# Optimization experiments

Hardware: AMD Instinct MI355X
Metric: run time of the kernel (lower is better)

The kernel has to match this reference:

```python
import jax, jax.numpy as jnp
import numpy as np

B, T, O, H, CTX, HOR = 32, 24, 128, 512, 256, 48
MAX_STEP = 2.0


def setup_inputs() -> dict:
    key = jax.random.key(0)
    ks = jax.random.split(key, 20)
    def lin(k, out_d, in_d):
        bound = 1.0 / np.sqrt(in_d)
        kw, kb = jax.random.split(k)
        W = jax.random.uniform(kw, (out_d, in_d), jnp.float32, -bound, bound)
        b = jax.random.uniform(kb, (out_d,), jnp.float32, -bound, bound)
        return W, b
    W_emb, b_emb = lin(ks[0], H, 2)
    W_ctx, b_ctx = lin(ks[1], H, CTX)
    Wi_enc, bi_enc = lin(ks[2], 3 * H, H)
    Wh_enc, bh_enc = lin(ks[3], 3 * H, H)
    Wi_cell, bi_cell = lin(ks[4], 3 * H, H)
    Wh_cell, bh_cell = lin(ks[5], 3 * H, H)
    W1, b1 = lin(ks[6], H, H)
    W2, b2 = lin(ks[7], 2, H)
    z_ctx = jax.random.normal(ks[8], (B, CTX), jnp.float32)
    traj_hist = jax.random.uniform(ks[9], (B, T, O, 2), jnp.float32) * 10.0
    return dict(z_ctx=z_ctx, traj_hist=traj_hist,
                W_emb=W_emb, b_emb=b_emb, W_ctx=W_ctx, b_ctx=b_ctx,
                Wi_enc=Wi_enc, Wh_enc=Wh_enc, bi_enc=bi_enc, bh_enc=bh_enc,
                Wi_cell=Wi_cell, Wh_cell=Wh_cell, bi_cell=bi_cell, bh_cell=bh_cell,
                W1=W1, b1=b1, W2=W2, b2=b2, horizon=HOR)


def _gru(h, x, Wi, Wh, bi, bh):
    # PyTorch GRU gate math: gates ordered (r, z, n)
    gi = x @ Wi.T + bi  # [N, 3H]
    gh = h @ Wh.T + bh
    ir, iz, inn = jnp.split(gi, 3, axis=-1)
    hr, hz, hn = jnp.split(gh, 3, axis=-1)
    r = jax.nn.sigmoid(ir + hr)
    z = jax.nn.sigmoid(iz + hz)
    n = jnp.tanh(inn + r * hn)
    return (1.0 - z) * n + z * h


def reference(z_ctx, traj_hist, W_emb, b_emb, W_ctx, b_ctx,
              Wi_enc, Wh_enc, bi_enc, bh_enc,
              Wi_cell, Wh_cell, bi_cell, bh_cell,
              W1, b1, W2, b2, horizon):
    b, t, o, _ = traj_hist.shape
    Hd = W_emb.shape[0]
    seq = traj_hist.transpose(0, 2, 1, 3).reshape(b * o, t, 2)  # [N, t, 2]
    emb = seq @ W_emb.T + b_emb  # [N, t, H]

    h0 = jnp.zeros((b * o, Hd), traj_hist.dtype)
    def enc_step(h, x):
        return _gru(h, x, Wi_enc, Wh_enc, bi_enc, bh_enc), None
    h, _ = jax.lax.scan(enc_step, h0, emb.transpose(1, 0, 2))

    ctx = z_ctx @ W_ctx.T + b_ctx                         # [b, H]
    ctx = jnp.repeat(ctx[:, None, :], o, axis=1).reshape(b * o, Hd)
    h = h + ctx

    state0 = seq[:, -1]  # [N, 2]
    def dec_step(carry, _):
        h, state = carry
        inp = state @ W_emb.T + b_emb
        h = _gru(h, inp, Wi_cell, Wh_cell, bi_cell, bh_cell)
        d = jax.nn.gelu(h @ W1.T + b1, approximate=False) @ W2.T + b2  # [N, 2]
        d = MAX_STEP * jnp.tanh(d / MAX_STEP)
        s = state + d
        state = jnp.stack([jnp.clip(s[..., 0], -90.0, 90.0),
                           jnp.mod(s[..., 1], 360.0)], axis=-1)
        return (h, state), state
    _, outs = jax.lax.scan(dec_step, (h, state0), None, length=horizon)
    # outs: [horizon, N, 2] -> [b, horizon, o, 2]
    return outs.transpose(1, 0, 2).reshape(b, o, horizon, 2).transpose(0, 2, 1, 3)
```

## Files before the change

kernel.cpp:

```cpp
#include <hip/hip_runtime.h>
#include <hip/hip_bf16.h>
#include <math.h>

#define BB 32
#define TT 24
#define OO 128
#define HH 512
#define CTXD 256
#define HOR 48
#define NN (BB*OO)
#define G3 (3*HH)
#define KS 17

typedef unsigned short ushortt;
typedef __attribute__((ext_vector_type(8))) short bf16x8;
typedef __attribute__((ext_vector_type(4))) float f32x4;

__device__ __forceinline__ ushortt f2bf(float x) {
    union { float f; unsigned u; } v; v.f = x;
    unsigned r = v.u + 0x7FFF + ((v.u >> 16) & 1);
    return (ushortt)(r >> 16);
}
__device__ __forceinline__ float bf2f(ushortt b) {
    union { unsigned u; float f; } v; v.u = ((unsigned)b) << 16;
    return v.f;
}
__device__ __forceinline__ void splitbf(float x, ushortt& hi, ushortt& lo) {
    hi = f2bf(x);
    lo = f2bf(x - bf2f(hi));
}
__device__ __forceinline__ float sigm(float x) { return 1.f / (1.f + __expf(-x)); }
__device__ __forceinline__ float tanh_fast(float x) {
    float xc = fminf(fmaxf(x, -10.f), 10.f);
    float e = __expf(2.f * xc);
    return (e - 1.f) / (e + 1.f);
}


#define STEP_LOADA(Ad, ksv) do { const unsigned ko = (unsigned)(ksv) * 512; \
  _Pragma("unroll") for (int m_ = 0; m_ < 2; m_++) { \
    Ad[m_*2+0] = *reinterpret_cast<const bf16x8*>(RAh + ao[m_] + ko); \
    Ad[m_*2+1] = *reinterpret_cast<const bf16x8*>(RAl + ao[m_] + ko); \
  } } while(0)
#define STEP_LOADB(Bd, ksv) do { const unsigned ko = (unsigned)(ksv) * 512; \
  _Pragma("unroll") for (int i_ = 0; i_ < 6; i_++) { \
    Bd[i_*2+0] = *reinterpret_cast<const bf16x8*>(Bh + bo[i_] + ko); \
    Bd[i_*2+1] = *reinterpret_cast<const bf16x8*>(Bl + bo[i_] + ko); \
  } } while(0)
#define STEP_MFMA(Av, Bv) do { \
  _Pragma("unroll") for (int m_ = 0; m_ < 2; m_++) \
  _Pragma("unroll") for (int i_ = 0; i_ < 6; i_++) \
    acc[m_][i_] = __builtin_amdgcn_mfma_f32_16x16x32_bf16(Av[m_*2+0], Bv[i_*2+0], acc[m_][i_], 0,0,0); \
  _Pragma("unroll") for (int m_ = 0; m_ < 2; m_++) \
  _Pragma("unroll") for (int i_ = 0; i_ < 6; i_++) \
    acc[m_][i_] = __builtin_amdgcn_mfma_f32_16x16x32_bf16(Av[m_*2+0], Bv[i_*2+1], acc[m_][i_], 0,0,0); \
  _Pragma("unroll") for (int m_ = 0; m_ < 2; m_++) \
  _Pragma("unroll") for (int i_ = 0; i_ < 6; i_++) \
    acc[m_][i_] = __builtin_amdgcn_mfma_f32_16x16x32_bf16(Av[m_*2+1], Bv[i_*2+0], acc[m_][i_], 0,0,0); \
  } while(0)

template<bool ENC>
__global__ __launch_bounds__(256, 2) void step_kernel(
    const ushortt* __restrict__ RAh, const ushortt* __restrict__ RAl,
    ushortt* __restrict__ WAh, ushortt* __restrict__ WAl,
    const ushortt* __restrict__ Bh, const ushortt* __restrict__ Bl,
    const float* __restrict__ U, const float* __restrict__ cin,
    const float* __restrict__ xsrc, int t, const float* __restrict__ ctx)
{
    __shared__ float hbuf[128 * 36];
    const int mb = blockIdx.x & 31;
    const int jb = blockIdx.x >> 5;
    const int w = threadIdx.x >> 6, lane = threadIdx.x & 63;
    const int quad = lane >> 4, l15 = lane & 15;
    const int mtg = mb * 8 + w * 2;

    f32x4 acc[2][6];
#pragma unroll
    for (int a = 0; a < 2; a++)
#pragma unroll
        for (int b = 0; b < 6; b++) acc[a][b] = (f32x4){0.f,0.f,0.f,0.f};

    unsigned ao[2], bo[6];
#pragma unroll
    for (int mt = 0; mt < 2; mt++) ao[mt] = (unsigned)(mtg + mt) * (KS*512) + lane * 8;
#pragma unroll
    for (int g = 0; g < 3; g++)
#pragma unroll
        for (int jt = 0; jt < 2; jt++)
            bo[g*2+jt] = (unsigned)(g*32 + jb*2 + jt) * (KS*512) + lane * 8;

    bf16x8 aC[4], bC[12], aN[4], bN[12];
    STEP_LOADA(aC, 0); STEP_LOADB(bC, 0);
#pragma unroll 1
    for (int ks = 0; ks < 16; ks += 2) {
        STEP_LOADA(aN, ks+1); STEP_LOADB(bN, ks+1);
        STEP_MFMA(aC, bC);
        STEP_LOADA(aC, ks+2); STEP_LOADB(bC, ks+2);
        STEP_MFMA(aN, bN);
    }
    STEP_MFMA(aC, bC);

    const int jlo = jb * 32;
    float u0[2], u1[2], cc[2];
#pragma unroll
    for (int jt = 0; jt < 2; jt++) {
        int j = jlo + jt*16 + l15;
        u0[jt] = U[(1024 + j) * 2];
        u1[jt] = U[(1024 + j) * 2 + 1];
        cc[jt] = cin[1024 + j];
    }
    float x0v[2][4], x1v[2][4];
#pragma unroll
    for (int mt = 0; mt < 2; mt++)
#pragma unroll
        for (int reg = 0; reg < 4; reg++) {
            int row = (mtg + mt) * 16 + quad * 4 + reg;
            const float* p;
            if (ENC) p = xsrc + (((size_t)(row >> 7) * TT + t) * OO + (row & 127)) * 2;
            else     p = xsrc + (size_t)row * 2;
            x0v[mt][reg] = p[0]; x1v[mt][reg] = p[1];
        }
#pragma unroll
    for (int mt = 0; mt < 2; mt++)
#pragma unroll
        for (int jt = 0; jt < 2; jt++) {
            int qk = jt*2 + (l15 >> 3), slot = l15 & 7;
#pragma unroll
            for (int reg = 0; reg < 4; reg++) {
                int row = (mtg + mt) * 16 + quad * 4 + reg;
                float pr = acc[mt][0*2+jt][reg];
                float pz = acc[mt][1*2+jt][reg];
                float hn = acc[mt][2*2+jt][reg];
                unsigned pos = ((unsigned)((mtg + mt) * KS + jb) * 64 + qk*16 + quad*4 + reg) * 8 + slot;
                float hold = bf2f(RAh[pos]) + bf2f(RAl[pos]);
                float inn = fmaf(x1v[mt][reg], u1[jt], fmaf(x0v[mt][reg], u0[jt], cc[jt]));
                float rg = sigm(pr), zg = sigm(pz);
                float nn = tanh_fast(inn + rg * hn);
                float h = (1.f - zg) * nn + zg * hold;
                if (ENC && t == TT - 1) h += ctx[(size_t)(row >> 7) * HH + jlo + jt*16 + l15];
                hbuf[(w*32 + mt*16 + quad*4 + reg) * 36 + jt*16 + l15] = h;
            }
        }
    __syncthreads();
#pragma unroll
    for (int rr = 0; rr < 2; rr++) {
        int fr = threadIdx.x + 256 * rr;
        int mt8 = fr >> 6, fl = fr & 63;
        int qk = fl >> 4, rloc = mt8 * 16 + (fl & 15);
        const float4 v0 = *reinterpret_cast<const float4*>(&hbuf[rloc * 36 + qk * 8]);
        const float4 v1 = *reinterpret_cast<const float4*>(&hbuf[rloc * 36 + qk * 8 + 4]);
        float src[8] = {v0.x, v0.y, v0.z, v0.w, v1.x, v1.y, v1.z, v1.w};
        bf16x8 hv, lv;
#pragma unroll
        for (int s = 0; s < 8; s++) {
            ushortt hi, lo; splitbf(src[s], hi, lo);
            hv[s] = (short)hi; lv[s] = (short)lo;
        }
        unsigned base = ((unsigned)((mb*8 + mt8) * KS + jb) * 64 + fl) * 8;
        *reinterpret_cast<bf16x8*>(WAh + base) = hv;
        *reinterpret_cast<bf16x8*>(WAl + base) = lv;
    }
    if (ENC && jb == 0 && threadIdx.x < 128) {
        int row = mb * 128 + threadIdx.x;
        int tn = (t < TT - 1) ? (t + 1) : (TT - 1);
        const float* p = xsrc + (((size_t)(row >> 7) * TT + tn) * OO + (row & 127)) * 2;
        ushortt h0, l0, h1, l1;
        splitbf(p[0], h0, l0); splitbf(p[1], h1, l1);
        unsigned xb = ((unsigned)((row >> 4) * KS + 16) * 64 + (row & 15)) * 8;
        WAh[xb + 0] = h0; WAl[xb + 0] = l0;
        WAh[xb + 1] = h1; WAl[xb + 1] = l1;
    }
}

#define HEAD_LOADA(Ad, ksv) do { const unsigned ko = (unsigned)(ksv) * 512; \
  _Pragma("unroll") for (int m_ = 0; m_ < 2; m_++) { \
    Ad[m_*2+0] = *reinterpret_cast<const bf16x8*>(Ah + hao[m_] + ko); \
    Ad[m_*2+1] = *reinterpret_cast<const bf16x8*>(Al + hao[m_] + ko); \
  } } while(0)
#define HEAD_LOADB(Bd, ksv) do { const unsigned ko = (unsigned)(ksv) * 512; \
  _Pragma("unroll") for (int n_ = 0; n_ < 2; n_++) { \
    Bd[n_*2+0] = *reinterpret_cast<const bf16x8*>(Bh + hbo[n_] + ko); \
    Bd[n_*2+1] = *reinterpret_cast<const bf16x8*>(Bl + hbo[n_] + ko); \
  } } while(0)
#define HEAD_MFMA(Av, Bv) do { \
  _Pragma("unroll") for (int m_ = 0; m_ < 2; m_++) \
  _Pragma("unroll") for (int n_ = 0; n_ < 2; n_++) { \
    acc[m_][n_] = __builtin_amdgcn_mfma_f32_16x16x32_bf16(Av[m_*2+0], Bv[n_*2+0], acc[m_][n_], 0,0,0); \
    acc[m_][n_] = __builtin_amdgcn_mfma_f32_16x16x32_bf16(Av[m_*2+0], Bv[n_*2+1], acc[m_][n_], 0,0,0); \
    acc[m_][n_] = __builtin_amdgcn_mfma_f32_16x16x32_bf16(Av[m_*2+1], Bv[n_*2+0], acc[m_][n_], 0,0,0); \
  } } while(0)

__global__ __launch_bounds__(256, 2) void head_kernel(
    ushortt* Ah, ushortt* Al,
    const ushortt* __restrict__ Bh, const ushortt* __restrict__ Bl,
    const float* __restrict__ W2, const float* __restrict__ b2,
    float* __restrict__ d, unsigned* __restrict__ ctr,
    float* state, float* __restrict__ out, int t)
{
    const int mb = blockIdx.x & 31;
    const int nb = blockIdx.x >> 5;
    const int w = threadIdx.x >> 6, lane = threadIdx.x & 63;
    const int quad = lane >> 4, l15 = lane & 15;
    const int mtg = mb * 8 + w * 2;

    f32x4 acc[2][2];
#pragma unroll
    for (int a = 0; a < 2; a++)
#pragma unroll
        for (int b = 0; b < 2; b++) acc[a][b] = (f32x4){0.f,0.f,0.f,0.f};

    unsigned hao[2], hbo[2];
#pragma unroll
    for (int mt = 0; mt < 2; mt++) hao[mt] = (unsigned)(mtg + mt) * (KS*512) + lane * 8;
#pragma unroll
    for (int nt = 0; nt < 2; nt++) hbo[nt] = (unsigned)(nb*2 + nt) * (KS*512) + lane * 8;

    bf16x8 aC[4], bC[4], aN[4], bN[4];
    HEAD_LOADA(aC, 0); HEAD_LOADB(bC, 0);
#pragma unroll 1
    for (int ks = 0; ks < 16; ks += 2) {
        HEAD_LOADA(aN, ks+1); HEAD_LOADB(bN, ks+1);
        HEAD_MFMA(aC, bC);
        HEAD_LOADA(aC, ks+2); HEAD_LOADB(bC, ks+2);
        HEAD_MFMA(aN, bN);
    }
    HEAD_MFMA(aC, bC);

    float w2a[2], w2b[2];
#pragma unroll
    for (int nt = 0; nt < 2; nt++) {
        int col = (nb*2 + nt) * 16 + l15;
        w2a[nt] = W2[col]; w2b[nt] = W2[HH + col];
    }
    float p0[2][4], p1[2][4];
#pragma unroll
    for (int mt = 0; mt < 2; mt++)
#pragma unroll
        for (int reg = 0; reg < 4; reg++) { p0[mt][reg] = 0.f; p1[mt][reg] = 0.f; }
#pragma unroll
    for (int mt = 0; mt < 2; mt++)
#pragma unroll
        for (int nt = 0; nt < 2; nt++)
#pragma unroll
            for (int reg = 0; reg < 4; reg++) {
                float v = acc[mt][nt][reg];
                v = 0.5f * v * (1.0f + erff(v * 0.70710678118654752440f));
                p0[mt][reg] = fmaf(v, w2a[nt], p0[mt][reg]);
                p1[mt][reg] = fmaf(v, w2b[nt], p1[mt][reg]);
            }
#pragma unroll
    for (int m = 1; m < 16; m <<= 1)
#pragma unroll
        for (int mt = 0; mt < 2; mt++)
#pragma unroll
            for (int reg = 0; reg < 4; reg++) {
                p0[mt][reg] += __shfl_xor(p0[mt][reg], m, 64);
                p1[mt][reg] += __shfl_xor(p1[mt][reg], m, 64);
            }
    if (l15 == 0) {
#pragma unroll
        for (int mt = 0; mt < 2; mt++)
#pragma unroll
            for (int reg = 0; reg < 4; reg++) {
                int row = (mtg + mt) * 16 + quad * 4 + reg;
                atomicAdd(&d[row * 2], p0[mt][reg]);
                atomicAdd(&d[row * 2 + 1], p1[mt][reg]);
            }
    }

    __syncthreads();
    __shared__ unsigned lastv;
    if (threadIdx.x == 0) lastv = atomicAdd(ctr, 1u);
    __syncthreads();
    if (lastv == 511) {
        __threadfence();
#pragma unroll 1
        for (int rr = 0; rr < 16; rr++) {
            int row = rr * 256 + threadIdx.x;
            float d0 = d[row * 2]     + b2[0];
            float d1 = d[row * 2 + 1] + b2[1];
            d0 = 2.0f * tanhf(d0 * 0.5f);
            d1 = 2.0f * tanhf(d1 * 0.5f);
            float s0 = state[row * 2] + d0;
            s0 = fminf(fmaxf(s0, -90.f), 90.f);
            float s1 = state[row * 2 + 1] + d1;
            float rrm = fmodf(s1, 360.f);
            if (rrm < 0.f) rrm += 360.f;
            state[row * 2] = s0; state[row * 2 + 1] = rrm;
            float* op = out + (((size_t)(row >> 7) * HOR + t) * OO + (row & 127)) * 2;
            op[0] = s0; op[1] = rrm;
            ushortt h0, l0, h1, l1;
            splitbf(s0, h0, l0); splitbf(rrm, h1, l1);
            unsigned xb = ((unsigned)((row >> 4) * KS + 16) * 64 + (row & 15)) * 8;
            Ah[xb + 0] = h0; Al[xb + 0] = l0;
            Ah[xb + 1] = h1; Al[xb + 1] = l1;
        }
    }
}

__global__ __launch_bounds__(256) void fuse_kernel(
    const float* __restrict__ Wi_enc, const float* __restrict__ bi_enc,
    const float* __restrict__ Wi_cell, const float* __restrict__ bi_cell,
    const float* __restrict__ W_emb, const float* __restrict__ b_emb,
    float* __restrict__ Ue, float* __restrict__ ce,
    float* __restrict__ Ud, float* __restrict__ cd) {
    int w = threadIdx.x >> 6, lane = threadIdx.x & 63;
    int gidx = blockIdx.x * 4 + w;
    int which = gidx >= G3;
    int j = gidx - which * G3;
    const float* Wi = which ? Wi_cell : Wi_enc;
    const float* bi = which ? bi_cell : bi_enc;
    float u0 = 0.f, u1 = 0.f, cc = 0.f;
#pragma unroll
    for (int i = 0; i < 8; i++) {
        int k = i * 64 + lane;
        float wv = Wi[(size_t)j * HH + k];
        u0 = fmaf(wv, W_emb[2*k],   u0);
        u1 = fmaf(wv, W_emb[2*k+1], u1);
        cc = fmaf(wv, b_emb[k],     cc);
    }
#pragma unroll
    for (int m = 1; m < 64; m <<= 1) {
        u0 += __shfl_xor(u0, m, 64);
        u1 += __shfl_xor(u1, m, 64);
        cc += __shfl_xor(cc, m, 64);
    }
    if (lane == 0) {
        float* Uo = which ? Ud : Ue;
        float* cv = which ? cd : ce;
        Uo[j * 2 + 0] = u0; Uo[j * 2 + 1] = u1; cv[j] = cc + bi[j];
    }
}

__global__ void pack_frag(const float* __restrict__ W, const float* __restrict__ bhv,
                          const float* __restrict__ U, const float* __restrict__ cin,
                          const float* __restrict__ b1,
                          ushortt* __restrict__ Fh, ushortt* __restrict__ Fl, int N) {
    int idx = blockIdx.x * 256 + threadIdx.x;
    if (idx >= N * KS * 4) return;
    int n = idx / (KS * 4);
    int rem = idx - n * (KS * 4);
    int ks = rem >> 2, quad = rem & 3;
    int nt = n >> 4, l15 = n & 15;
    ushortt hv[8], lv[8];
#pragma unroll
    for (int s = 0; s < 8; s++) {
        int k = ks * 32 + quad * 8 + s;
        float v = 0.f;
        if (k < 512) v = W[(size_t)n * 512 + k];
        else if (k == 512) v = (U && n < 1024) ? U[n * 2 + 0] : 0.f;
        else if (k == 513) v = (U && n < 1024) ? U[n * 2 + 1] : 0.f;
        else if (k == 514) v = U ? ((n < 1024) ? (cin[n] + bhv[n]) : bhv[n]) : b1[n];
        ushortt hi, lo; splitbf(v, hi, lo);
        hv[s] = hi; lv[s] = lo;
    }
    size_t pos = ((size_t)(nt * KS + ks) * 64 + quad * 16 + l15) * 8;
#pragma unroll
    for (int s = 0; s < 8; s++) { Fh[pos + s] = hv[s]; Fl[pos + s] = lv[s]; }
}

__global__ void ctx_kernel(const float* __restrict__ z, const float* __restrict__ Wc,
                           const float* __restrict__ bc, float* __restrict__ ctx) {
    int idx = blockIdx.x * 256 + threadIdx.x;
    int b = idx >> 9, j = idx & 511;
    float acc = bc[j];
    const float4* zp = (const float4*)(z + (size_t)b * CTXD);
    const float4* wp = (const float4*)(Wc + (size_t)j * CTXD);
    for (int k = 0; k < CTXD / 4; k++) {
        float4 a = zp[k], ww = wp[k];
        acc = fmaf(a.x, ww.x, fmaf(a.y, ww.y, fmaf(a.z, ww.z, fmaf(a.w, ww.w, acc))));
    }
    ctx[idx] = acc;
}

__global__ void init_kernel(const float* __restrict__ traj,
                            ushortt* __restrict__ Ah0, ushortt* __restrict__ Al0,
                            ushortt* __restrict__ Ah1, ushortt* __restrict__ Al1,
                            float* __restrict__ state, float* __restrict__ d,
                            unsigned* __restrict__ ctr) {
    int b = blockIdx.x;
    if (b < 1024) {
        int item = b * 256 + threadIdx.x;
        int mt = item >> 10, ks = (item >> 6) & 15, q4 = item & 63;
        size_t pos32 = ((size_t)(mt * KS + ks)) * 256 + q4 * 4;
        uint4 z = {0u,0u,0u,0u};
        *reinterpret_cast<uint4*>(((unsigned*)Ah0) + pos32) = z;
        *reinterpret_cast<uint4*>(((unsigned*)Al0) + pos32) = z;
    } else if (b < 1040) {
        int row = (b - 1024) * 256 + threadIdx.x;
        int bi = row >> 7, o = row & 127;
        const float* tp = traj + (((size_t)bi * TT + 0) * OO + o) * 2;
        ushortt xh0, xl0, xh1, xl1;
        splitbf(tp[0], xh0, xl0); splitbf(tp[1], xh1, xl1);
        for (int qk = 0; qk < 4; qk++)
            for (int slot = 0; slot < 8; slot++) {
                size_t p = (((size_t)(row >> 4) * KS + 16) * 64 + qk * 16 + (row & 15)) * 8 + slot;
                ushortt vh0 = 0, vl0 = 0, vh1 = 0;
                if (qk == 0 && slot == 0) { vh0 = xh0; vl0 = xl0; }
                else if (qk == 0 && slot == 1) { vh0 = xh1; vl0 = xl1; }
                else if (qk == 0 && slot == 2) { vh0 = 0x3F80; vh1 = 0x3F80; }
                Ah0[p] = vh0; Al0[p] = vl0; Ah1[p] = vh1; Al1[p] = 0;
            }
        const float* sp = traj + (((size_t)bi * TT + 23) * OO + o) * 2;
        state[row * 2] = sp[0]; state[row * 2 + 1] = sp[1];
    } else if (b < 1424) {
        int i = (b - 1040) * 256 + threadIdx.x;
        float4 z = {0.f,0.f,0.f,0.f};
        reinterpret_cast<float4*>(d)[i] = z;
    } else {
        if (threadIdx.x < 48) ctr[threadIdx.x] = 0u;
    }
}

extern "C" void kernel_launch(void* const* d_in, const int* in_sizes, int n_in,
                              void* d_out, int out_size, void* d_ws, size_t ws_size,
                              hipStream_t stream) {
    const float* z_ctx   = (const float*)d_in[0];
    const float* traj    = (const float*)d_in[1];
    const float* W_emb   = (const float*)d_in[2];
    const float* b_emb   = (const float*)d_in[3];
    const float* W_ctx   = (const float*)d_in[4];
    const float* b_ctx   = (const float*)d_in[5];
    const float* Wi_enc  = (const float*)d_in[6];
    const float* Wh_enc  = (const float*)d_in[7];
    const float* bi_enc  = (const float*)d_in[8];
    const float* bh_enc  = (const float*)d_in[9];
    const float* Wi_cell = (const float*)d_in[10];
    const float* Wh_cell = (const float*)d_in[11];
    const float* bi_cell = (const float*)d_in[12];
    const float* bh_cell = (const float*)d_in[13];
    const float* W1      = (const float*)d_in[14];
    const float* b1      = (const float*)d_in[15];
    const float* W2      = (const float*)d_in[16];
    const float* b2      = (const float*)d_in[17];
    float* out = (float*)d_out;

    char* ws = (char*)d_ws;
    size_t off = 0;
    auto alloc = [&](size_t bytes) { void* p = ws + off; off += (bytes + 255) & ~(size_t)255; return p; };
    const size_t hfrag = (size_t)256 * KS * 512 * 2;
    const size_t wfrag = (size_t)96  * KS * 512 * 2;
    const size_t w1frag = (size_t)32 * KS * 512 * 2;
    ushortt* Ah0 = (ushortt*)alloc(hfrag);
    ushortt* Al0 = (ushortt*)alloc(hfrag);
    ushortt* Ah1 = (ushortt*)alloc(hfrag);
    ushortt* Al1 = (ushortt*)alloc(hfrag);
    ushortt* WheH = (ushortt*)alloc(wfrag);
    ushortt* WheL = (ushortt*)alloc(wfrag);
    ushortt* WhdH = (ushortt*)alloc(wfrag);
    ushortt* WhdL = (ushortt*)alloc(wfrag);
    ushortt* W1H  = (ushortt*)alloc(w1frag);
    ushortt* W1L  = (ushortt*)alloc(w1frag);
    float*   state = (float*)alloc((size_t)NN * 2 * 4);
    float*   ctxb  = (float*)alloc((size_t)BB * HH * 4);
    float*   Ue    = (float*)alloc((size_t)G3 * 2 * 4);
    float*   ce    = (float*)alloc((size_t)G3 * 4);
    float*   Ud    = (float*)alloc((size_t)G3 * 2 * 4);
    float*   cd    = (float*)alloc((size_t)G3 * 4);
    float*   dbuf  = (float*)alloc((size_t)HOR * NN * 2 * 4);
    unsigned* ctr  = (unsigned*)alloc(HOR * 4);

    ushortt* bufAh[2] = {Ah0, Ah1};
    ushortt* bufAl[2] = {Al0, Al1};

    fuse_kernel<<<768, 256, 0, stream>>>(Wi_enc, bi_enc, Wi_cell, bi_cell,
                                         W_emb, b_emb, Ue, ce, Ud, cd);
    ctx_kernel<<<(BB * HH) / 256, 256, 0, stream>>>(z_ctx, W_ctx, b_ctx, ctxb);
    pack_frag<<<(G3 * KS * 4 + 255) / 256, 256, 0, stream>>>(Wh_enc, bh_enc, Ue, ce, nullptr, WheH, WheL, G3);
    pack_frag<<<(G3 * KS * 4 + 255) / 256, 256, 0, stream>>>(Wh_cell, bh_cell, Ud, cd, nullptr, WhdH, WhdL, G3);
    pack_frag<<<(HH * KS * 4 + 255) / 256, 256, 0, stream>>>(W1, nullptr, nullptr, nullptr, b1, W1H, W1L, HH);
    init_kernel<<<1425, 256, 0, stream>>>(traj, Ah0, Al0, Ah1, Al1, state, dbuf, ctr);

    for (int t = 0; t < TT; t++) {
        int rp = t & 1, wp = (t + 1) & 1;
        step_kernel<true><<<512, 256, 0, stream>>>(bufAh[rp], bufAl[rp], bufAh[wp], bufAl[wp],
                                                   WheH, WheL, Ue, ce, traj, t, ctxb);
    }
    for (int t = 0; t < HOR; t++) {
        int s = TT + t;
        int rp = s & 1, wp = (s + 1) & 1;
        step_kernel<false><<<512, 256, 0, stream>>>(bufAh[rp], bufAl[rp], bufAh[wp], bufAl[wp],
                                                    WhdH, WhdL, Ud, cd, state, t, nullptr);
        head_kernel<<<512, 256, 0, stream>>>(bufAh[wp], bufAl[wp], W1H, W1L, W2, b2,
                                             dbuf + (size_t)t * NN * 2, ctr + t, state, out, t);
    }
}
```

Before: 3.501 ms.

## Fuse all GRU steps into one persistent kernel with per-batch group barriers

Replaces the 120 per-step launches of the step and head kernels with a single persistent kernel. Blocks loop over all encoder and decoder steps and synchronise through atomic counters, one counter per group of 16 blocks sharing a batch row slab. The input projection and biases move out of the augmented K tile (17 tiles become 16) into per-column register FMAs, and the decoder state lives in shared memory. Prep kernels are merged into one launch. This removes launch overhead and global round-trips, but it depends on all 512 blocks being co-resident at two blocks per CU, and spin-waiting adds latency to every step.

```diff
diff --git a/kernel.cpp b/kernel.cpp
--- a/kernel.cpp
+++ b/kernel.cpp
@@ -10,7 +10,8 @@
 #define HOR 48
 #define NN (BB*OO)
 #define G3 (3*HH)
-#define KS 17
+#define KS2 16
+#define TILE_U16 (KS2*512)
 
 typedef unsigned short ushortt;
 typedef __attribute__((ext_vector_type(8))) short bf16x8;
@@ -36,18 +37,29 @@
     return (e - 1.f) / (e + 1.f);
 }
 
-
-#define STEP_LOADA(Ad, ksv) do { const unsigned ko = (unsigned)(ksv) * 512; \
+__device__ __forceinline__ void group_barrier(unsigned* cnt, unsigned target) {
+    __syncthreads();
+    if (threadIdx.x == 0) {
+        __hip_atomic_fetch_add(cnt, 1u, __ATOMIC_RELEASE, __HIP_MEMORY_SCOPE_AGENT);
+        while (__hip_atomic_load(cnt, __ATOMIC_RELAXED, __HIP_MEMORY_SCOPE_AGENT) < target)
+            __builtin_amdgcn_s_sleep(2);
+        (void)__hip_atomic_load(cnt, __ATOMIC_ACQUIRE, __HIP_MEMORY_SCOPE_AGENT);
+    }
+    __syncthreads();
+}
+
+
+#define MLOADA(Ad, ksv) do { const unsigned ko = (unsigned)(ksv) * 512; \
   _Pragma("unroll") for (int m_ = 0; m_ < 2; m_++) { \
     Ad[m_*2+0] = *reinterpret_cast<const bf16x8*>(RAh + ao[m_] + ko); \
     Ad[m_*2+1] = *reinterpret_cast<const bf16x8*>(RAl + ao[m_] + ko); \
   } } while(0)
-#define STEP_LOADB(Bd, ksv) do { const unsigned ko = (unsigned)(ksv) * 512; \
+#define MLOADB(Bd, ksv) do { const unsigned ko = (unsigned)(ksv) * 512; \
   _Pragma("unroll") for (int i_ = 0; i_ < 6; i_++) { \
     Bd[i_*2+0] = *reinterpret_cast<const bf16x8*>(Bh + bo[i_] + ko); \
     Bd[i_*2+1] = *reinterpret_cast<const bf16x8*>(Bl + bo[i_] + ko); \
   } } while(0)
-#define STEP_MFMA(Av, Bv) do { \
+#define MMFMA(Av, Bv) do { \
   _Pragma("unroll") for (int m_ = 0; m_ < 2; m_++) \
   _Pragma("unroll") for (int i_ = 0; i_ < 6; i_++) \
     acc[m_][i_] = __builtin_amdgcn_mfma_f32_16x16x32_bf16(Av[m_*2+0], Bv[i_*2+0], acc[m_][i_], 0,0,0); \
@@ -59,356 +71,355 @@
     acc[m_][i_] = __builtin_amdgcn_mfma_f32_16x16x32_bf16(Av[m_*2+1], Bv[i_*2+0], acc[m_][i_], 0,0,0); \
   } while(0)
 
-template<bool ENC>
-__global__ __launch_bounds__(256, 2) void step_kernel(
-    const ushortt* __restrict__ RAh, const ushortt* __restrict__ RAl,
-    ushortt* __restrict__ WAh, ushortt* __restrict__ WAl,
-    const ushortt* __restrict__ Bh, const ushortt* __restrict__ Bl,
-    const float* __restrict__ U, const float* __restrict__ cin,
-    const float* __restrict__ xsrc, int t, const float* __restrict__ ctx)
+#define HLOADA(Ad, ksv) do { const unsigned ko = (unsigned)(ksv) * 512; \
+  _Pragma("unroll") for (int m_ = 0; m_ < 2; m_++) { \
+    Ad[m_*2+0] = *reinterpret_cast<const bf16x8*>(WAh + ao[m_] + ko); \
+    Ad[m_*2+1] = *reinterpret_cast<const bf16x8*>(WAl + ao[m_] + ko); \
+  } } while(0)
+#define HLOADB(Bd, ksv) do { const unsigned ko = (unsigned)(ksv) * 512; \
+  _Pragma("unroll") for (int n_ = 0; n_ < 2; n_++) { \
+    Bd[n_*2+0] = *reinterpret_cast<const bf16x8*>(W1H + bo1[n_] + ko); \
+    Bd[n_*2+1] = *reinterpret_cast<const bf16x8*>(W1L + bo1[n_] + ko); \
+  } } while(0)
+#define HMFMA(Av, Bv) do { \
+  _Pragma("unroll") for (int m_ = 0; m_ < 2; m_++) \
+  _Pragma("unroll") for (int n_ = 0; n_ < 2; n_++) { \
+    hacc[m_][n_] = __builtin_amdgcn_mfma_f32_16x16x32_bf16(Av[m_*2+0], Bv[n_*2+0], hacc[m_][n_], 0,0,0); \
+    hacc[m_][n_] = __builtin_amdgcn_mfma_f32_16x16x32_bf16(Av[m_*2+0], Bv[n_*2+1], hacc[m_][n_], 0,0,0); \
+    hacc[m_][n_] = __builtin_amdgcn_mfma_f32_16x16x32_bf16(Av[m_*2+1], Bv[n_*2+0], hacc[m_][n_], 0,0,0); \
+  } } while(0)
+
+__global__ __launch_bounds__(256, 2) void main_kernel(
+    ushortt* Ah0, ushortt* Al0, ushortt* Ah1, ushortt* Al1,
+    const ushortt* __restrict__ WheH, const ushortt* __restrict__ WheL,
+    const ushortt* __restrict__ WhdH, const ushortt* __restrict__ WhdL,
+    const ushortt* __restrict__ W1H,  const ushortt* __restrict__ W1L,
+    const float* __restrict__ Ue, const float* __restrict__ ce,
+    const float* __restrict__ Ud, const float* __restrict__ cd,
+    const float* __restrict__ bhe, const float* __restrict__ bhd,
+    const float* __restrict__ traj, const float* __restrict__ ctx,
+    const float* __restrict__ b1v, const float* __restrict__ W2,
+    const float* __restrict__ b2v, float* __restrict__ dpart,
+    unsigned* bar, float* __restrict__ out)
 {
     __shared__ float hbuf[128 * 36];
+    __shared__ float sstate[128 * 2];
     const int mb = blockIdx.x & 31;
     const int jb = blockIdx.x >> 5;
     const int w = threadIdx.x >> 6, lane = threadIdx.x & 63;
     const int quad = lane >> 4, l15 = lane & 15;
     const int mtg = mb * 8 + w * 2;
-
-    f32x4 acc[2][6];
-#pragma unroll
-    for (int a = 0; a < 2; a++)
-#pragma unroll
-        for (int b = 0; b < 6; b++) acc[a][b] = (f32x4){0.f,0.f,0.f,0.f};
-
-    unsigned ao[2], bo[6];
-#pragma unroll
-    for (int mt = 0; mt < 2; mt++) ao[mt] = (unsigned)(mtg + mt) * (KS*512) + lane * 8;
+    const int jlo = jb * 32;
+    unsigned* grpcnt = bar + mb * 16;
+    unsigned tgt = 0;
+
+    ushortt* bh_[2] = {Ah0, Ah1};
+    ushortt* bl_[2] = {Al0, Al1};
+
+    unsigned ao[2], bo[6], bo1[2];
+#pragma unroll
+    for (int mt = 0; mt < 2; mt++) ao[mt] = (unsigned)(mtg + mt) * TILE_U16 + lane * 8;
 #pragma unroll
     for (int g = 0; g < 3; g++)
 #pragma unroll
         for (int jt = 0; jt < 2; jt++)
-            bo[g*2+jt] = (unsigned)(g*32 + jb*2 + jt) * (KS*512) + lane * 8;
-
-    bf16x8 aC[4], bC[12], aN[4], bN[12];
-    STEP_LOADA(aC, 0); STEP_LOADB(bC, 0);
+            bo[g*2+jt] = (unsigned)(g*32 + jb*2 + jt) * TILE_U16 + lane * 8;
+#pragma unroll
+    for (int nt = 0; nt < 2; nt++) bo1[nt] = (unsigned)(jb*2 + nt) * TILE_U16 + lane * 8;
+
+    float b1r[2], w2a[2], w2b[2];
+#pragma unroll
+    for (int nt = 0; nt < 2; nt++) {
+        int col = jlo + nt*16 + l15;
+        b1r[nt] = b1v[col]; w2a[nt] = W2[col]; w2b[nt] = W2[HH + col];
+    }
+    const float b20 = b2v[0], b21 = b2v[1];
+
+    float Ur0[2],Ur1[2],Uz0[2],Uz1[2],Un0[2],Un1[2],Crr[2],Czz[2],bhn[2],cinn[2];
+
 #pragma unroll 1
-    for (int ks = 0; ks < 16; ks += 2) {
-        STEP_LOADA(aN, ks+1); STEP_LOADB(bN, ks+1);
-        STEP_MFMA(aC, bC);
-        STEP_LOADA(aC, ks+2); STEP_LOADB(bC, ks+2);
-        STEP_MFMA(aN, bN);
+    for (int s = 0; s < TT + HOR; s++) {
+        const bool enc = s < TT;
+        if (s == 0 || s == TT) {
+            const float* U  = enc ? Ue : Ud;
+            const float* ci = enc ? ce : cd;
+            const float* bh = enc ? bhe : bhd;
+#pragma unroll
+            for (int jt = 0; jt < 2; jt++) {
+                int j = jlo + jt*16 + l15;
+                Ur0[jt] = U[j*2];            Ur1[jt] = U[j*2+1];
+                Uz0[jt] = U[(512+j)*2];      Uz1[jt] = U[(512+j)*2+1];
+                Un0[jt] = U[(1024+j)*2];     Un1[jt] = U[(1024+j)*2+1];
+                Crr[jt] = ci[j] + bh[j];
+                Czz[jt] = ci[512+j] + bh[512+j];
+                cinn[jt] = ci[1024+j];       bhn[jt] = bh[1024+j];
+            }
+            if (!enc) {
+                if (threadIdx.x < 128) {
+                    int lrow = threadIdx.x;
+                    const float* sp = traj + (((size_t)mb * TT + 23) * OO + lrow) * 2;
+                    sstate[lrow*2] = sp[0]; sstate[lrow*2+1] = sp[1];
+                }
+                __syncthreads();
+            }
+        }
+        const ushortt* RAh = bh_[s & 1];
+        const ushortt* RAl = bl_[s & 1];
+        ushortt* WAh = bh_[(s + 1) & 1];
+        ushortt* WAl = bl_[(s + 1) & 1];
+        const ushortt* Bh = enc ? WheH : WhdH;
+        const ushortt* Bl = enc ? WheL : WhdL;
+
+        f32x4 acc[2][6];
+#pragma unroll
+        for (int a = 0; a < 2; a++)
+#pragma unroll
+            for (int b = 0; b < 6; b++) acc[a][b] = (f32x4){0.f,0.f,0.f,0.f};
+
+        if (s > 0) {
+            bf16x8 aC[4], bC[12], aN[4], bN[12];
+            MLOADA(aC, 0); MLOADB(bC, 0);
+#pragma unroll 1
+            for (int ks = 0; ks < 14; ks += 2) {
+                MLOADA(aN, ks+1); MLOADB(bN, ks+1);
+                MMFMA(aC, bC);
+                MLOADA(aC, ks+2); MLOADB(bC, ks+2);
+                MMFMA(aN, bN);
+            }
+            MLOADA(aN, 15); MLOADB(bN, 15);
+            MMFMA(aC, bC);
+            MMFMA(aN, bN);
+        }
+
+        float x0v[2][4], x1v[2][4];
+#pragma unroll
+        for (int mt = 0; mt < 2; mt++)
+#pragma unroll
+            for (int reg = 0; reg < 4; reg++) {
+                int lrow = (w*2 + mt) * 16 + quad * 4 + reg;
+                if (enc) {
+                    const float* p = traj + (((size_t)mb * TT + s) * OO + lrow) * 2;
+                    x0v[mt][reg] = p[0]; x1v[mt][reg] = p[1];
+                } else {
+                    x0v[mt][reg] = sstate[lrow*2]; x1v[mt][reg] = sstate[lrow*2+1];
+                }
+            }
+
+#pragma unroll
+        for (int mt = 0; mt < 2; mt++)
+#pragma unroll
+            for (int jt = 0; jt < 2; jt++) {
+                int qk = jt*2 + (l15 >> 3), slot = l15 & 7;
+#pragma unroll
+                for (int reg = 0; reg < 4; reg++) {
+                    float x0 = x0v[mt][reg], x1 = x1v[mt][reg];
+                    float pr = acc[mt][0+jt][reg] + fmaf(x1, Ur1[jt], fmaf(x0, Ur0[jt], Crr[jt]));
+                    float pz = acc[mt][2+jt][reg] + fmaf(x1, Uz1[jt], fmaf(x0, Uz0[jt], Czz[jt]));
+                    float hn = acc[mt][4+jt][reg] + bhn[jt];
+                    float inn = fmaf(x1, Un1[jt], fmaf(x0, Un0[jt], cinn[jt]));
+                    float hold = 0.f;
+                    if (s > 0) {
+                        unsigned pos = (unsigned)(mtg + mt) * TILE_U16 + (unsigned)jb * 512
+                                     + (unsigned)(qk*16 + quad*4 + reg) * 8 + slot;
+                        hold = bf2f(RAh[pos]) + bf2f(RAl[pos]);
+                    }
+                    float rg = sigm(pr), zg = sigm(pz);
+                    float nn = tanh_fast(inn + rg * hn);
+                    float h = (1.f - zg) * nn + zg * hold;
+                    if (enc && s == TT - 1)
+                        h += ctx[(size_t)mb * HH + jlo + jt*16 + l15];
+                    hbuf[(w*32 + mt*16 + quad*4 + reg) * 36 + jt*16 + l15] = h;
+                }
+            }
+        __syncthreads();
+#pragma unroll
+        for (int rr = 0; rr < 2; rr++) {
+            int fr = threadIdx.x + 256 * rr;
+            int mt8 = fr >> 6, fl = fr & 63;
+            int qk = fl >> 4, rloc = mt8 * 16 + (fl & 15);
+            const float4 v0 = *reinterpret_cast<const float4*>(&hbuf[rloc * 36 + qk * 8]);
+            const float4 v1 = *reinterpret_cast<const float4*>(&hbuf[rloc * 36 + qk * 8 + 4]);
+            float src[8] = {v0.x, v0.y, v0.z, v0.w, v1.x, v1.y, v1.z, v1.w};
+            bf16x8 hv, lv;
+#pragma unroll
+            for (int q = 0; q < 8; q++) {
+                ushortt hi, lo; splitbf(src[q], hi, lo);
+                hv[q] = (short)hi; lv[q] = (short)lo;
+            }
+            unsigned base = (unsigned)(mb*8 + mt8) * TILE_U16 + (unsigned)jb * 512 + fl * 8;
+            *reinterpret_cast<bf16x8*>(WAh + base) = hv;
+            *reinterpret_cast<bf16x8*>(WAl + base) = lv;
+        }
+        __syncthreads();
+
+        tgt += 16;
+        group_barrier(grpcnt, tgt);
+
+        if (!enc) {
+            f32x4 hacc[2][2];
+#pragma unroll
+            for (int a = 0; a < 2; a++)
+#pragma unroll
+                for (int b = 0; b < 2; b++) hacc[a][b] = (f32x4){0.f,0.f,0.f,0.f};
+            {
+                bf16x8 aC[4], bC[4], aN[4], bN[4];
+                HLOADA(aC, 0); HLOADB(bC, 0);
+#pragma unroll 1
+                for (int ks = 0; ks < 14; ks += 2) {
+                    HLOADA(aN, ks+1); HLOADB(bN, ks+1);
+                    HMFMA(aC, bC);
+                    HLOADA(aC, ks+2); HLOADB(bC, ks+2);
+                    HMFMA(aN, bN);
+                }
+                HLOADA(aN, 15); HLOADB(bN, 15);
+                HMFMA(aC, bC);
+                HMFMA(aN, bN);
+            }
+            float p0[2][4], p1[2][4];
+#pragma unroll
+            for (int mt = 0; mt < 2; mt++)
+#pragma unroll
+                for (int reg = 0; reg < 4; reg++) { p0[mt][reg] = 0.f; p1[mt][reg] = 0.f; }
+#pragma unroll
+            for (int mt = 0; mt < 2; mt++)
+#pragma unroll
+                for (int nt = 0; nt < 2; nt++)
+#pragma unroll
+                    for (int reg = 0; reg < 4; reg++) {
+                        float v = hacc[mt][nt][reg] + b1r[nt];
+                        v = 0.5f * v * (1.0f + erff(v * 0.70710678118654752440f));
+                        p0[mt][reg] = fmaf(v, w2a[nt], p0[mt][reg]);
+                        p1[mt][reg] = fmaf(v, w2b[nt], p1[mt][reg]);
+                    }
+#pragma unroll
+            for (int m = 1; m < 16; m <<= 1)
+#pragma unroll
+                for (int mt = 0; mt < 2; mt++)
+#pragma unroll
+                    for (int reg = 0; reg < 4; reg++) {
+                        p0[mt][reg] += __shfl_xor(p0[mt][reg], m, 64);
+                        p1[mt][reg] += __shfl_xor(p1[mt][reg], m, 64);
+                    }
+            if (l15 == 0) {
+#pragma unroll
+                for (int mt = 0; mt < 2; mt++)
+#pragma unroll
+                    for (int reg = 0; reg < 4; reg++) {
+                        int lrow = (w*2 + mt) * 16 + quad * 4 + reg;
+                        float* dp = dpart + ((size_t)(mb*16 + jb) * 128 + lrow) * 2;
+                        dp[0] = p0[mt][reg]; dp[1] = p1[mt][reg];
+                    }
+            }
+            tgt += 16;
+            group_barrier(grpcnt, tgt);
+            if (threadIdx.x < 128) {
+                int lrow = threadIdx.x;
+                float d0 = 0.f, d1 = 0.f;
+#pragma unroll
+                for (int j2 = 0; j2 < 16; j2++) {
+                    const float* dp = dpart + ((size_t)(mb*16 + j2) * 128 + lrow) * 2;
+                    d0 += dp[0]; d1 += dp[1];
+                }
+                d0 += b20; d1 += b21;
+                d0 = 2.0f * tanhf(d0 * 0.5f);
+                d1 = 2.0f * tanhf(d1 * 0.5f);
+                float s0 = sstate[lrow*2] + d0;
+                s0 = fminf(fmaxf(s0, -90.f), 90.f);
+                float s1 = sstate[lrow*2+1] + d1;
+                float rrm = fmodf(s1, 360.f);
+                if (rrm < 0.f) rrm += 360.f;
+                sstate[lrow*2] = s0; sstate[lrow*2+1] = rrm;
+                if (jb == 0) {
+                    float* op = out + (((size_t)mb * HOR + (s - TT)) * OO + lrow) * 2;
+                    op[0] = s0; op[1] = rrm;
+                }
+            }
+            __syncthreads();
+        }
     }
-    STEP_MFMA(aC, bC);
-
-    const int jlo = jb * 32;
-    float u0[2], u1[2], cc[2];
-#pragma unroll
-    for (int jt = 0; jt < 2; jt++) {
-        int j = jlo + jt*16 + l15;
-        u0[jt] = U[(1024 + j) * 2];
-        u1[jt] = U[(1024 + j) * 2 + 1];
-        cc[jt] = cin[1024 + j];
+}
+
+__device__ __forceinline__ void pack16(const float* __restrict__ W,
+                                       ushortt* __restrict__ Fh, ushortt* __restrict__ Fl,
+                                       int item) {
+    int n = item >> 6, rem = item & 63;
+    int ks = rem >> 2, quadk = rem & 3;
+    int nt = n >> 4, l15 = n & 15;
+    ushortt hv[8], lv[8];
+#pragma unroll
+    for (int q = 0; q < 8; q++) {
+        float v = W[(size_t)n * 512 + ks*32 + quadk*8 + q];
+        ushortt hi, lo; splitbf(v, hi, lo);
+        hv[q] = hi; lv[q] = lo;
     }
-    float x0v[2][4], x1v[2][4];
-#pragma unroll
-    for (int mt = 0; mt < 2; mt++)
-#pragma unroll
-        for (int reg = 0; reg < 4; reg++) {
-            int row = (mtg + mt) * 16 + quad * 4 + reg;
-            const float* p;
-            if (ENC) p = xsrc + (((size_t)(row >> 7) * TT + t) * OO + (row & 127)) * 2;
-            else     p = xsrc + (size_t)row * 2;
-            x0v[mt][reg] = p[0]; x1v[mt][reg] = p[1];
-        }
-#pragma unroll
-    for (int mt = 0; mt < 2; mt++)
-#pragma unroll
-        for (int jt = 0; jt < 2; jt++) {
-            int qk = jt*2 + (l15 >> 3), slot = l15 & 7;
-#pragma unroll
-            for (int reg = 0; reg < 4; reg++) {
-                int row = (mtg + mt) * 16 + quad * 4 + reg;
-                float pr = acc[mt][0*2+jt][reg];
-                float pz = acc[mt][1*2+jt][reg];
-                float hn = acc[mt][2*2+jt][reg];
-                unsigned pos = ((unsigned)((mtg + mt) * KS + jb) * 64 + qk*16 + quad*4 + reg) * 8 + slot;
-                float hold = bf2f(RAh[pos]) + bf2f(RAl[pos]);
-                float inn = fmaf(x1v[mt][reg], u1[jt], fmaf(x0v[mt][reg], u0[jt], cc[jt]));
-                float rg = sigm(pr), zg = sigm(pz);
-                float nn = tanh_fast(inn + rg * hn);
-                float h = (1.f - zg) * nn + zg * hold;
-                if (ENC && t == TT - 1) h += ctx[(size_t)(row >> 7) * HH + jlo + jt*16 + l15];
-                hbuf[(w*32 + mt*16 + quad*4 + reg) * 36 + jt*16 + l15] = h;
-            }
-        }
-    __syncthreads();
-#pragma unroll
-    for (int rr = 0; rr < 2; rr++) {
-        int fr = threadIdx.x + 256 * rr;
-        int mt8 = fr >> 6, fl = fr & 63;
-        int qk = fl >> 4, rloc = mt8 * 16 + (fl & 15);
-        const float4 v0 = *reinterpret_cast<const float4*>(&hbuf[rloc * 36 + qk * 8]);
-        const float4 v1 = *reinterpret_cast<const float4*>(&hbuf[rloc * 36 + qk * 8 + 4]);
-        float src[8] = {v0.x, v0.y, v0.z, v0.w, v1.x, v1.y, v1.z, v1.w};
-        bf16x8 hv, lv;
-#pragma unroll
-        for (int s = 0; s < 8; s++) {
-            ushortt hi, lo; splitbf(src[s], hi, lo);
-            hv[s] = (short)hi; lv[s] = (short)lo;
-        }
-        unsigned base = ((unsigned)((mb*8 + mt8) * KS + jb) * 64 + fl) * 8;
-        *reinterpret_cast<bf16x8*>(WAh + base) = hv;
-        *reinterpret_cast<bf16x8*>(WAl + base) = lv;
-    }
-    if (ENC && jb == 0 && threadIdx.x < 128) {
-        int row = mb * 128 + threadIdx.x;
-        int tn = (t < TT - 1) ? (t + 1) : (TT - 1);
-        const float* p = xsrc + (((size_t)(row >> 7) * TT + tn) * OO + (row & 127)) * 2;
-        ushortt h0, l0, h1, l1;
-        splitbf(p[0], h0, l0); splitbf(p[1], h1, l1);
-        unsigned xb = ((unsigned)((row >> 4) * KS + 16) * 64 + (row & 15)) * 8;
-        WAh[xb + 0] = h0; WAl[xb + 0] = l0;
-        WAh[xb + 1] = h1; WAl[xb + 1] = l1;
-    }
-}
-
-#define HEAD_LOADA(Ad, ksv) do { const unsigned ko = (unsigned)(ksv) * 512; \
-  _Pragma("unroll") for (int m_ = 0; m_ < 2; m_++) { \
-    Ad[m_*2+0] = *reinterpret_cast<const bf16x8*>(Ah + hao[m_] + ko); \
-    Ad[m_*2+1] = *reinterpret_cast<const bf16x8*>(Al + hao[m_] + ko); \
-  } } while(0)
-#define HEAD_LOADB(Bd, ksv) do { const unsigned ko = (unsigned)(ksv) * 512; \
-  _Pragma("unroll") for (int n_ = 0; n_ < 2; n_++) { \
-    Bd[n_*2+0] = *reinterpret_cast<const bf16x8*>(Bh + hbo[n_] + ko); \
-    Bd[n_*2+1] = *reinterpret_cast<const bf16x8*>(Bl + hbo[n_] + ko); \
-  } } while(0)
-#define HEAD_MFMA(Av, Bv) do { \
-  _Pragma("unroll") for (int m_ = 0; m_ < 2; m_++) \
-  _Pragma("unroll") for (int n_ = 0; n_ < 2; n_++) { \
-    acc[m_][n_] = __builtin_amdgcn_mfma_f32_16x16x32_bf16(Av[m_*2+0], Bv[n_*2+0], acc[m_][n_], 0,0,0); \
-    acc[m_][n_] = __builtin_amdgcn_mfma_f32_16x16x32_bf16(Av[m_*2+0], Bv[n_*2+1], acc[m_][n_], 0,0,0); \
-    acc[m_][n_] = __builtin_amdgcn_mfma_f32_16x16x32_bf16(Av[m_*2+1], Bv[n_*2+0], acc[m_][n_], 0,0,0); \
-  } } while(0)
-
-__global__ __launch_bounds__(256, 2) void head_kernel(
-    ushortt* Ah, ushortt* Al,
-    const ushortt* __restrict__ Bh, const ushortt* __restrict__ Bl,
-    const float* __restrict__ W2, const float* __restrict__ b2,
-    float* __restrict__ d, unsigned* __restrict__ ctr,
-    float* state, float* __restrict__ out, int t)
-{
-    const int mb = blockIdx.x & 31;
-    const int nb = blockIdx.x >> 5;
-    const int w = threadIdx.x >> 6, lane = threadIdx.x & 63;
-    const int quad = lane >> 4, l15 = lane & 15;
-    const int mtg = mb * 8 + w * 2;
-
-    f32x4 acc[2][2];
-#pragma unroll
-    for (int a = 0; a < 2; a++)
-#pragma unroll
-        for (int b = 0; b < 2; b++) acc[a][b] = (f32x4){0.f,0.f,0.f,0.f};
-
-    unsigned hao[2], hbo[2];
-#pragma unroll
-    for (int mt = 0; mt < 2; mt++) hao[mt] = (unsigned)(mtg + mt) * (KS*512) + lane * 8;
-#pragma unroll
-    for (int nt = 0; nt < 2; nt++) hbo[nt] = (unsigned)(nb*2 + nt) * (KS*512) + lane * 8;
-
-    bf16x8 aC[4], bC[4], aN[4], bN[4];
-    HEAD_LOADA(aC, 0); HEAD_LOADB(bC, 0);
-#pragma unroll 1
-    for (int ks = 0; ks < 16; ks += 2) {
-        HEAD_LOADA(aN, ks+1); HEAD_LOADB(bN, ks+1);
-        HEAD_MFMA(aC, bC);
-        HEAD_LOADA(aC, ks+2); HEAD_LOADB(bC, ks+2);
-        HEAD_MFMA(aN, bN);
-    }
-    HEAD_MFMA(aC, bC);
-
-    float w2a[2], w2b[2];
-#pragma unroll
-    for (int nt = 0; nt < 2; nt++) {
-        int col = (nb*2 + nt) * 16 + l15;
-        w2a[nt] = W2[col]; w2b[nt] = W2[HH + col];
-    }
-    float p0[2][4], p1[2][4];
-#pragma unroll
-    for (int mt = 0; mt < 2; mt++)
-#pragma unroll
-        for (int reg = 0; reg < 4; reg++) { p0[mt][reg] = 0.f; p1[mt][reg] = 0.f; }
-#pragma unroll
-    for (int mt = 0; mt < 2; mt++)
-#pragma unroll
-        for (int nt = 0; nt < 2; nt++)
-#pragma unroll
-            for (int reg = 0; reg < 4; reg++) {
-                float v = acc[mt][nt][reg];
-                v = 0.5f * v * (1.0f + erff(v * 0.70710678118654752440f));
-                p0[mt][reg] = fmaf(v, w2a[nt], p0[mt][reg]);
-                p1[mt][reg] = fmaf(v, w2b[nt], p1[mt][reg]);
-            }
-#pragma unroll
-    for (int m = 1; m < 16; m <<= 1)
-#pragma unroll
-        for (int mt = 0; mt < 2; mt++)
-#pragma unroll
-            for (int reg = 0; reg < 4; reg++) {
-                p0[mt][reg] += __shfl_xor(p0[mt][reg], m, 64);
-                p1[mt][reg] += __shfl_xor(p1[mt][reg], m, 64);
-            }
-    if (l15 == 0) {
-#pragma unroll
-        for (int mt = 0; mt < 2; mt++)
-#pragma unroll
-            for (int reg = 0; reg < 4; reg++) {
-                int row = (mtg + mt) * 16 + quad * 4 + reg;
-                atomicAdd(&d[row * 2], p0[mt][reg]);
-                atomicAdd(&d[row * 2 + 1], p1[mt][reg]);
-            }
-    }
-
-    __syncthreads();
-    __shared__ unsigned lastv;
-    if (threadIdx.x == 0) lastv = atomicAdd(ctr, 1u);
-    __syncthreads();
-    if (lastv == 511) {
-        __threadfence();
-#pragma unroll 1
-        for (int rr = 0; rr < 16; rr++) {
-            int row = rr * 256 + threadIdx.x;
-            float d0 = d[row * 2]     + b2[0];
-            float d1 = d[row * 2 + 1] + b2[1];
-            d0 = 2.0f * tanhf(d0 * 0.5f);
-            d1 = 2.0f * tanhf(d1 * 0.5f);
-            float s0 = state[row * 2] + d0;
-            s0 = fminf(fmaxf(s0, -90.f), 90.f);
-            float s1 = state[row * 2 + 1] + d1;
-            float rrm = fmodf(s1, 360.f);
-            if (rrm < 0.f) rrm += 360.f;
-            state[row * 2] = s0; state[row * 2 + 1] = rrm;
-            float* op = out + (((size_t)(row >> 7) * HOR + t) * OO + (row & 127)) * 2;
-            op[0] = s0; op[1] = rrm;
-            ushortt h0, l0, h1, l1;
-            splitbf(s0, h0, l0); splitbf(rrm, h1, l1);
-            unsigned xb = ((unsigned)((row >> 4) * KS + 16) * 64 + (row & 15)) * 8;
-            Ah[xb + 0] = h0; Al[xb + 0] = l0;
-            Ah[xb + 1] = h1; Al[xb + 1] = l1;
-        }
-    }
-}
-
-__global__ __launch_bounds__(256) void fuse_kernel(
+    size_t pos = ((size_t)nt * TILE_U16) + (size_t)ks * 512 + (quadk*16 + l15) * 8;
+#pragma unroll
+    for (int q = 0; q < 8; q++) { Fh[pos + q] = hv[q]; Fl[pos + q] = lv[q]; }
+}
+
+__global__ __launch_bounds__(256) void prep_kernel(
+    const float* __restrict__ Wh_enc, const float* __restrict__ Wh_cell,
+    const float* __restrict__ W1,
     const float* __restrict__ Wi_enc, const float* __restrict__ bi_enc,
     const float* __restrict__ Wi_cell, const float* __restrict__ bi_cell,
     const float* __restrict__ W_emb, const float* __restrict__ b_emb,
+    const float* __restrict__ z, const float* __restrict__ Wc, const float* __restrict__ bc,
+    ushortt* __restrict__ WheH, ushortt* __restrict__ WheL,
+    ushortt* __restrict__ WhdH, ushortt* __restrict__ WhdL,
+    ushortt* __restrict__ W1H, ushortt* __restrict__ W1L,
     float* __restrict__ Ue, float* __restrict__ ce,
-    float* __restrict__ Ud, float* __restrict__ cd) {
-    int w = threadIdx.x >> 6, lane = threadIdx.x & 63;
-    int gidx = blockIdx.x * 4 + w;
-    int which = gidx >= G3;
-    int j = gidx - which * G3;
-    const float* Wi = which ? Wi_cell : Wi_enc;
-    const float* bi = which ? bi_cell : bi_enc;
-    float u0 = 0.f, u1 = 0.f, cc = 0.f;
-#pragma unroll
-    for (int i = 0; i < 8; i++) {
-        int k = i * 64 + lane;
-        float wv = Wi[(size_t)j * HH + k];
-        u0 = fmaf(wv, W_emb[2*k],   u0);
-        u1 = fmaf(wv, W_emb[2*k+1], u1);
-        cc = fmaf(wv, b_emb[k],     cc);
-    }
-#pragma unroll
-    for (int m = 1; m < 64; m <<= 1) {
-        u0 += __shfl_xor(u0, m, 64);
-        u1 += __shfl_xor(u1, m, 64);
-        cc += __shfl_xor(cc, m, 64);
-    }
-    if (lane == 0) {
-        float* Uo = which ? Ud : Ue;
-        float* cv = which ? cd : ce;
-        Uo[j * 2 + 0] = u0; Uo[j * 2 + 1] = u1; cv[j] = cc + bi[j];
-    }
-}
-
-__global__ void pack_frag(const float* __restrict__ W, const float* __restrict__ bhv,
-                          const float* __restrict__ U, const float* __restrict__ cin,
-                          const float* __restrict__ b1,
-                          ushortt* __restrict__ Fh, ushortt* __restrict__ Fl, int N) {
-    int idx = blockIdx.x * 256 + threadIdx.x;
-    if (idx >= N * KS * 4) return;
-    int n = idx / (KS * 4);
-    int rem = idx - n * (KS * 4);
-    int ks = rem >> 2, quad = rem & 3;
-    int nt = n >> 4, l15 = n & 15;
-    ushortt hv[8], lv[8];
-#pragma unroll
-    for (int s = 0; s < 8; s++) {
-        int k = ks * 32 + quad * 8 + s;
-        float v = 0.f;
-        if (k < 512) v = W[(size_t)n * 512 + k];
-        else if (k == 512) v = (U && n < 1024) ? U[n * 2 + 0] : 0.f;
-        else if (k == 513) v = (U && n < 1024) ? U[n * 2 + 1] : 0.f;
-        else if (k == 514) v = U ? ((n < 1024) ? (cin[n] + bhv[n]) : bhv[n]) : b1[n];
-        ushortt hi, lo; splitbf(v, hi, lo);
-        hv[s] = hi; lv[s] = lo;
-    }
-    size_t pos = ((size_t)(nt * KS + ks) * 64 + quad * 16 + l15) * 8;
-#pragma unroll
-    for (int s = 0; s < 8; s++) { Fh[pos + s] = hv[s]; Fl[pos + s] = lv[s]; }
-}
-
-__global__ void ctx_kernel(const float* __restrict__ z, const float* __restrict__ Wc,
-                           const float* __restrict__ bc, float* __restrict__ ctx) {
-    int idx = blockIdx.x * 256 + threadIdx.x;
-    int b = idx >> 9, j = idx & 511;
-    float acc = bc[j];
-    const float4* zp = (const float4*)(z + (size_t)b * CTXD);
-    const float4* wp = (const float4*)(Wc + (size_t)j * CTXD);
-    for (int k = 0; k < CTXD / 4; k++) {
-        float4 a = zp[k], ww = wp[k];
-        acc = fmaf(a.x, ww.x, fmaf(a.y, ww.y, fmaf(a.z, ww.z, fmaf(a.w, ww.w, acc))));
-    }
-    ctx[idx] = acc;
-}
-
-__global__ void init_kernel(const float* __restrict__ traj,
-                            ushortt* __restrict__ Ah0, ushortt* __restrict__ Al0,
-                            ushortt* __restrict__ Ah1, ushortt* __restrict__ Al1,
-                            float* __restrict__ state, float* __restrict__ d,
-                            unsigned* __restrict__ ctr) {
+    float* __restrict__ Ud, float* __restrict__ cd,
+    float* __restrict__ ctx, unsigned* __restrict__ bar)
+{
     int b = blockIdx.x;
-    if (b < 1024) {
-        int item = b * 256 + threadIdx.x;
-        int mt = item >> 10, ks = (item >> 6) & 15, q4 = item & 63;
-        size_t pos32 = ((size_t)(mt * KS + ks)) * 256 + q4 * 4;
-        uint4 z = {0u,0u,0u,0u};
-        *reinterpret_cast<uint4*>(((unsigned*)Ah0) + pos32) = z;
-        *reinterpret_cast<uint4*>(((unsigned*)Al0) + pos32) = z;
-    } else if (b < 1040) {
-        int row = (b - 1024) * 256 + threadIdx.x;
-        int bi = row >> 7, o = row & 127;
-        const float* tp = traj + (((size_t)bi * TT + 0) * OO + o) * 2;
-        ushortt xh0, xl0, xh1, xl1;
-        splitbf(tp[0], xh0, xl0); splitbf(tp[1], xh1, xl1);
-        for (int qk = 0; qk < 4; qk++)
-            for (int slot = 0; slot < 8; slot++) {
-                size_t p = (((size_t)(row >> 4) * KS + 16) * 64 + qk * 16 + (row & 15)) * 8 + slot;
-                ushortt vh0 = 0, vl0 = 0, vh1 = 0;
-                if (qk == 0 && slot == 0) { vh0 = xh0; vl0 = xl0; }
-                else if (qk == 0 && slot == 1) { vh0 = xh1; vl0 = xl1; }
-                else if (qk == 0 && slot == 2) { vh0 = 0x3F80; vh1 = 0x3F80; }
-                Ah0[p] = vh0; Al0[p] = vl0; Ah1[p] = vh1; Al1[p] = 0;
-            }
-        const float* sp = traj + (((size_t)bi * TT + 23) * OO + o) * 2;
-        state[row * 2] = sp[0]; state[row * 2 + 1] = sp[1];
-    } else if (b < 1424) {
-        int i = (b - 1040) * 256 + threadIdx.x;
-        float4 z = {0.f,0.f,0.f,0.f};
-        reinterpret_cast<float4*>(d)[i] = z;
+    if (b < 384) {
+        pack16(Wh_enc, WheH, WheL, b * 256 + threadIdx.x);
+    } else if (b < 768) {
+        pack16(Wh_cell, WhdH, WhdL, (b - 384) * 256 + threadIdx.x);
+    } else if (b < 896) {
+        pack16(W1, W1H, W1L, (b - 768) * 256 + threadIdx.x);
+    } else if (b < 1664) {
+        int w = threadIdx.x >> 6, lane = threadIdx.x & 63;
+        int gidx = (b - 896) * 4 + w;
+        int which = gidx >= G3;
+        int j = gidx - which * G3;
+        const float* Wi = which ? Wi_cell : Wi_enc;
+        const float* bi = which ? bi_cell : bi_enc;
+        float u0 = 0.f, u1 = 0.f, cc = 0.f;
+#pragma unroll
+        for (int i = 0; i < 8; i++) {
+            int k = i * 64 + lane;
+            float wv = Wi[(size_t)j * HH + k];
+            u0 = fmaf(wv, W_emb[2*k],   u0);
+            u1 = fmaf(wv, W_emb[2*k+1], u1);
+            cc = fmaf(wv, b_emb[k],     cc);
+        }
+#pragma unroll
+        for (int m = 1; m < 64; m <<= 1) {
+            u0 += __shfl_xor(u0, m, 64);
+            u1 += __shfl_xor(u1, m, 64);
+            cc += __shfl_xor(cc, m, 64);
+        }
+        if (lane == 0) {
+            float* Uo = which ? Ud : Ue;
+            float* cv = which ? cd : ce;
+            Uo[j*2] = u0; Uo[j*2+1] = u1; cv[j] = cc + bi[j];
+        }
+    } else if (b < 1728) {
+        int idx = (b - 1664) * 256 + threadIdx.x;
+        int bb = idx >> 9, j = idx & 511;
+        float acc = bc[j];
+        const float4* zp = (const float4*)(z + (size_t)bb * CTXD);
+        const float4* wp = (const float4*)(Wc + (size_t)j * CTXD);
+#pragma unroll 4
+        for (int k = 0; k < CTXD / 4; k++) {
+            float4 a = zp[k], ww = wp[k];
+            acc = fmaf(a.x, ww.x, fmaf(a.y, ww.y, fmaf(a.z, ww.z, fmaf(a.w, ww.w, acc))));
+        }
+        ctx[idx] = acc;
     } else {
-        if (threadIdx.x < 48) ctr[threadIdx.x] = 0u;
+        bar[threadIdx.x] = 0u;
+        bar[threadIdx.x + 256] = 0u;
     }
 }
 
@@ -438,9 +449,9 @@
     char* ws = (char*)d_ws;
     size_t off = 0;
     auto alloc = [&](size_t bytes) { void* p = ws + off; off += (bytes + 255) & ~(size_t)255; return p; };
-    const size_t hfrag = (size_t)256 * KS * 512 * 2;
-    const size_t wfrag = (size_t)96  * KS * 512 * 2;
-    const size_t w1frag = (size_t)32 * KS * 512 * 2;
+    const size_t hfrag  = (size_t)256 * TILE_U16 * 2;
+    const size_t wfrag  = (size_t)96  * TILE_U16 * 2;
+    const size_t w1frag = (size_t)32  * TILE_U16 * 2;
     ushortt* Ah0 = (ushortt*)alloc(hfrag);
     ushortt* Al0 = (ushortt*)alloc(hfrag);
     ushortt* Ah1 = (ushortt*)alloc(hfrag);
@@ -451,37 +462,23 @@
     ushortt* WhdL = (ushortt*)alloc(wfrag);
     ushortt* W1H  = (ushortt*)alloc(w1frag);
     ushortt* W1L  = (ushortt*)alloc(w1frag);
-    float*   state = (float*)alloc((size_t)NN * 2 * 4);
-    float*   ctxb  = (float*)alloc((size_t)BB * HH * 4);
-    float*   Ue    = (float*)alloc((size_t)G3 * 2 * 4);
-    float*   ce    = (float*)alloc((size_t)G3 * 4);
-    float*   Ud    = (float*)alloc((size_t)G3 * 2 * 4);
-    float*   cd    = (float*)alloc((size_t)G3 * 4);
-    float*   dbuf  = (float*)alloc((size_t)HOR * NN * 2 * 4);
-    unsigned* ctr  = (unsigned*)alloc(HOR * 4);
-
-    ushortt* bufAh[2] = {Ah0, Ah1};
-    ushortt* bufAl[2] = {Al0, Al1};
-
-    fuse_kernel<<<768, 256, 0, stream>>>(Wi_enc, bi_enc, Wi_cell, bi_cell,
-                                         W_emb, b_emb, Ue, ce, Ud, cd);
-    ctx_kernel<<<(BB * HH) / 256, 256, 0, stream>>>(z_ctx, W_ctx, b_ctx, ctxb);
-    pack_frag<<<(G3 * KS * 4 + 255) / 256, 256, 0, stream>>>(Wh_enc, bh_enc, Ue, ce, nullptr, WheH, WheL, G3);
-    pack_frag<<<(G3 * KS * 4 + 255) / 256, 256, 0, stream>>>(Wh_cell, bh_cell, Ud, cd, nullptr, WhdH, WhdL, G3);
-    pack_frag<<<(HH * KS * 4 + 255) / 256, 256, 0, stream>>>(W1, nullptr, nullptr, nullptr, b1, W1H, W1L, HH);
-    init_kernel<<<1425, 256, 0, stream>>>(traj, Ah0, Al0, Ah1, Al1, state, dbuf, ctr);
-
-    for (int t = 0; t < TT; t++) {
-        int rp = t & 1, wp = (t + 1) & 1;
-        step_kernel<true><<<512, 256, 0, stream>>>(bufAh[rp], bufAl[rp], bufAh[wp], bufAl[wp],
-                                                   WheH, WheL, Ue, ce, traj, t, ctxb);
-    }
-    for (int t = 0; t < HOR; t++) {
-        int s = TT + t;
-        int rp = s & 1, wp = (s + 1) & 1;
-        step_kernel<false><<<512, 256, 0, stream>>>(bufAh[rp], bufAl[rp], bufAh[wp], bufAl[wp],
-                                                    WhdH, WhdL, Ud, cd, state, t, nullptr);
-        head_kernel<<<512, 256, 0, stream>>>(bufAh[wp], bufAl[wp], W1H, W1L, W2, b2,
-                                             dbuf + (size_t)t * NN * 2, ctr + t, state, out, t);
-    }
-}
+    float*   Ue   = (float*)alloc((size_t)G3 * 2 * 4);
+    float*   ce   = (float*)alloc((size_t)G3 * 4);
+    float*   Ud   = (float*)alloc((size_t)G3 * 2 * 4);
+    float*   cd   = (float*)alloc((size_t)G3 * 4);
+    float*   ctxb = (float*)alloc((size_t)BB * HH * 4);
+    float*   dpart = (float*)alloc((size_t)32 * 16 * 128 * 2 * 4);
+    unsigned* bar  = (unsigned*)alloc(512 * 4);
+
+    prep_kernel<<<1729, 256, 0, stream>>>(Wh_enc, Wh_cell, W1,
+                                          Wi_enc, bi_enc, Wi_cell, bi_cell,
+                                          W_emb, b_emb, z_ctx, W_ctx, b_ctx,
+                                          WheH, WheL, WhdH, WhdL, W1H, W1L,
+                                          Ue, ce, Ud, cd, ctxb, bar);
+
+    main_kernel<<<512, 256, 0, stream>>>(Ah0, Al0, Ah1, Al1,
+                                         WheH, WheL, WhdH, WhdL, W1H, W1L,
+                                         Ue, ce, Ud, cd, bh_enc, bh_cell,
+                                         traj, ctxb, b1, W2, b2,
+                                         dpart, bar, out);
+}
```

Result: slower. 5.076 ms (+45.0%).
